# Optimization experiments

Hardware: AMD Instinct MI355X
Metric: run time of the kernel (lower is better)

## Reference

```python
import jax, jax.numpy as jnp
import numpy as np

TOP_K = 3
THRESH = 0.2
# scales=[1] -> multi_scale_fft reduces to one full-length window:
# combined_amplitudes = |rfft(x, axis=1)|.mean(channels)

def setup_inputs() -> dict:
    key = jax.random.key(0)
    x = jax.random.normal(key, (64, 4096, 64), dtype=jnp.float32)
    return {"x": x}

def _autocorr_score(xi, p):
    # xi: [T, C]; p: scalar int32 period (guaranteed in [2, T//2]).
    # Equivalent to mean over consecutive period-segments i of
    # cosine_similarity(flatten(seg_i), flatten(seg_{i+1})) — computed via
    # prefix sums of lag-p cross products so the segment reshape never needs
    # a data-dependent shape.
    T, C = xi.shape
    t = jnp.arange(T)
    tp = t + p
    m = (tp < T).astype(xi.dtype)
    xs = xi[jnp.clip(tp, 0, T - 1)]                  # [T, C] rows shifted by p
    r = (xi * xs).sum(-1) * m                        # <x[t], x[t+p]>
    q = (xi * xi).sum(-1)                            # ||x[t]||^2
    z = jnp.zeros((1,), xi.dtype)
    CR = jnp.concatenate([z, jnp.cumsum(r)])         # [T+1]
    CQ = jnp.concatenate([z, jnp.cumsum(q)])
    nper = T // p
    i = jnp.arange(T // 2)                           # max possible segments (p>=2)
    seg = i < (nper - 1)
    s = jnp.clip(i * p, 0, T)
    e = jnp.clip((i + 1) * p, 0, T)
    e2 = jnp.clip((i + 2) * p, 0, T)
    dots = CR[e] - CR[s]                             # flat dot(seg_i, seg_{i+1})
    na = jnp.sqrt(jnp.maximum(CQ[e] - CQ[s], 0.0))
    nb = jnp.sqrt(jnp.maximum(CQ[e2] - CQ[e], 0.0))
    cos = dots / jnp.maximum(na * nb, 1e-8)          # F.cosine_similarity eps
    denom = jnp.maximum(nper - 1, 1).astype(xi.dtype)
    score = jnp.where(seg, cos, 0.0).sum() / denom
    return jnp.where(nper >= 2, score, 0.0)

def reference(x):
    B, T, C = x.shape
    half = T // 2
    # multi-scale FFT with scales=[1]: single window == full sequence
    amps = jnp.abs(jnp.fft.rfft(x, axis=1)).mean(-1)       # [B, T//2+1]
    _, idx = jax.lax.top_k(amps, 2 * TOP_K)                 # [B, 2K]
    period_f = T / (idx + 1).astype(jnp.float32)            # candidate periods
    in_range = (period_f >= 2.0) & (period_f <= half)       # float-period filter
    p_int = jnp.clip(jnp.floor(period_f).astype(jnp.int32), 2, half)
    pf_floor = jnp.floor(period_f)
    in_range_int = (pf_floor >= 2.0) & (pf_floor <= half)   # int-period filter
    # autocorrelation validation score per (batch, candidate)
    scores = jax.vmap(lambda xi, ps: jax.vmap(lambda p: _autocorr_score(xi, p))(ps))(x, p_int)  # [B, 2K]
    valid = in_range & in_range_int & (scores > THRESH)
    # deterministic fallback periods (torch.randint branch unreachable for TOP_K=3)
    common = np.array([T // 4, T // 3, T // 2, int(T / 1.5)], dtype=np.int32)
    common = common[(common >= 2) & (common <= half)]
    add = jnp.asarray(common)                               # [>= TOP_K]

    def select(p_row, v_row):
        order = jnp.argsort(jnp.logical_not(v_row), stable=True)  # valid first, order kept
        sp = p_row[order][:TOP_K]
        cnt = jnp.minimum(v_row.sum(), TOP_K)
        j = jnp.arange(TOP_K)
        filled = jnp.where(j < cnt, sp, add[jnp.clip(j - cnt, 0, add.shape[0] - 1)])
        w = jnp.where(j < cnt, 1.0, 0.5)
        return filled.astype(jnp.float32), w.astype(jnp.float32)

    periods, weights = jax.vmap(select)(p_int, valid)       # [B, TOP_K] each
    return periods, weights
```

## Files before the change

kernel.cpp:

```cpp
#include <hip/hip_runtime.h>
#include <math.h>

#define T_LEN 4096
#define C_CH 64
#define B_N 64
#define NBINS 2049
#define K2 6
#define TOPK 3
#define THRESH_V 0.2f

#define PIDX(i) ((i) + ((i) >> 5))
#define ZSZ (T_LEN + (T_LEN >> 5))

__device__ __forceinline__ unsigned short f2bf(float v) {
    unsigned int u = __float_as_uint(v);
    u += 0x7FFFu + ((u >> 16) & 1u);
    return (unsigned short)(u >> 16);
}
__device__ __forceinline__ float bf2f(unsigned short h) {
    return __uint_as_float(((unsigned int)h) << 16);
}

__device__ __forceinline__ float2 cmul(float2 a, float2 b) {
    return make_float2(a.x * b.x - a.y * b.y, a.x * b.y + a.y * b.x);
}
__device__ __forceinline__ float2 cadd(float2 a, float2 b) { return make_float2(a.x + b.x, a.y + b.y); }
__device__ __forceinline__ float2 csub(float2 a, float2 b) { return make_float2(a.x - b.x, a.y - b.y); }

__device__ __forceinline__ void dft16(float2* v) {
    const float C2 = 0.70710678118654752f;
    const float C1 = 0.92387953251128676f;
    const float S1 = 0.38268343236508977f;
    const int br[16] = {0, 8, 4, 12, 2, 10, 6, 14, 1, 9, 5, 13, 3, 11, 7, 15};
    float2 a[16];
#pragma unroll
    for (int i = 0; i < 16; ++i) a[i] = v[br[i]];
#pragma unroll
    for (int g = 0; g < 16; g += 2) {
        float2 t = a[g + 1];
        a[g + 1] = csub(a[g], t);
        a[g] = cadd(a[g], t);
    }
#pragma unroll
    for (int g = 0; g < 16; g += 4) {
        {
            float2 t = a[g + 2];
            a[g + 2] = csub(a[g], t);
            a[g] = cadd(a[g], t);
        }
        {
            float2 t = make_float2(a[g + 3].y, -a[g + 3].x);
            a[g + 3] = csub(a[g + 1], t);
            a[g + 1] = cadd(a[g + 1], t);
        }
    }
    {
        const float2 W4[4] = {{1.f, 0.f}, {C2, -C2}, {0.f, -1.f}, {-C2, -C2}};
#pragma unroll
        for (int g = 0; g < 16; g += 8)
#pragma unroll
            for (int j = 0; j < 4; ++j) {
                float2 t = cmul(W4[j], a[g + 4 + j]);
                a[g + 4 + j] = csub(a[g + j], t);
                a[g + j] = cadd(a[g + j], t);
            }
    }
    {
        const float2 W8[8] = {{1.f, 0.f}, {C1, -S1}, {C2, -C2}, {S1, -C1},
                              {0.f, -1.f}, {-S1, -C1}, {-C2, -C2}, {-C1, -S1}};
#pragma unroll
        for (int j = 0; j < 8; ++j) {
            float2 t = cmul(W8[j], a[8 + j]);
            a[8 + j] = csub(a[j], t);
            a[j] = cadd(a[j], t);
        }
    }
#pragma unroll
    for (int i = 0; i < 16; ++i) v[i] = a[i];
}

__global__ void transpose_cvt_kernel(const float* __restrict__ x,
                                     unsigned short* __restrict__ xtbf,
                                     float* __restrict__ amps) {
    __shared__ float tile[64][65];
    const int b = blockIdx.y;
    const int t0 = blockIdx.x * 64;
    const int lane = threadIdx.x & 63;
    const int w = threadIdx.x >> 6;
    {
        const int blin = blockIdx.y * (T_LEN / 64) + blockIdx.x;
        if (threadIdx.x < 34) {
            int idx = blin * 34 + threadIdx.x;
            if (idx < B_N * NBINS) amps[idx] = 0.f;
        }
    }
    const float* xb = x + (size_t)b * T_LEN * C_CH;
#pragma unroll
    for (int i = 0; i < 16; ++i) {
        int r = w * 16 + i;
        tile[r][lane] = xb[(size_t)(t0 + r) * C_CH + lane];
    }
    __syncthreads();
    const int half = lane >> 5;
    const int tc = (lane & 31) * 2;
#pragma unroll
    for (int it = 0; it < 8; ++it) {
        int c = it * 8 + w * 2 + half;
        float v0 = tile[tc][c];
        float v1 = tile[tc + 1][c];
        unsigned int o = (unsigned int)f2bf(v0) | ((unsigned int)f2bf(v1) << 16);
        unsigned int* dst = (unsigned int*)(xtbf + ((size_t)b * C_CH + c) * T_LEN + t0);
        dst[lane & 31] = o;
    }
}

template <int MODE>
__global__ void fft_amp_kernel(const void* __restrict__ srcv, float* __restrict__ amps) {
    __shared__ float2 Z[ZSZ];
    const int pair = blockIdx.x;
    const int b = blockIdx.y;
    const int tid = threadIdx.x;

    if (MODE == 0) {
        const unsigned short* r0 =
            (const unsigned short*)srcv + ((size_t)b * C_CH + pair * 2) * T_LEN;
        const unsigned short* r1 = r0 + T_LEN;
#pragma unroll
        for (int k = 0; k < 2; ++k) {
            int t0 = k * 2048 + tid * 8;
            uint4 u0 = *(const uint4*)(r0 + t0);
            uint4 u1 = *(const uint4*)(r1 + t0);
            unsigned int a[4] = {u0.x, u0.y, u0.z, u0.w};
            unsigned int c[4] = {u1.x, u1.y, u1.z, u1.w};
#pragma unroll
            for (int j = 0; j < 4; ++j) {
                Z[PIDX(t0 + 2 * j)] = make_float2(__uint_as_float(a[j] << 16),
                                                  __uint_as_float(c[j] << 16));
                Z[PIDX(t0 + 2 * j + 1)] = make_float2(__uint_as_float(a[j] & 0xFFFF0000u),
                                                      __uint_as_float(c[j] & 0xFFFF0000u));
            }
        }
    } else {
        const float* x = (const float*)srcv;
        const int c0 = pair * 2;
        for (int t = tid; t < T_LEN; t += 256)
            Z[PIDX(t)] = *(const float2*)(x + ((size_t)b * T_LEN + t) * C_CH + c0);
    }
    __syncthreads();

    {
        float2 v[16];
#pragma unroll
        for (int t = 0; t < 16; ++t) v[t] = Z[PIDX(tid + 256 * t)];
        dft16(v);
        float s, c;
        __sincosf(-(float)tid * 1.5339807878856412e-3f, &s, &c);
        float2 w1 = make_float2(c, s), w = w1;
#pragma unroll
        for (int r = 1; r < 16; ++r) {
            v[r] = cmul(v[r], w);
            w = cmul(w, w1);
        }
#pragma unroll
        for (int r = 0; r < 16; ++r) Z[PIDX(256 * r + tid)] = v[r];
    }
    __syncthreads();

    {
        const int r = tid >> 4, mu = tid & 15;
        float2 v[16];
#pragma unroll
        for (int nu = 0; nu < 16; ++nu) v[nu] = Z[PIDX(256 * r + mu + 16 * nu)];
        dft16(v);
        float s, c;
        __sincosf(-(float)mu * 2.4543692606170259e-2f, &s, &c);
        float2 w1 = make_float2(c, s), w = w1;
#pragma unroll
        for (int rho = 1; rho < 16; ++rho) {
            v[rho] = cmul(v[rho], w);
            w = cmul(w, w1);
        }
#pragma unroll
        for (int rho = 0; rho < 16; ++rho) Z[PIDX(256 * r + mu + 16 * rho)] = v[rho];
    }
    __builtin_amdgcn_wave_barrier();

    {
        const int r = tid >> 4, rho = tid & 15;
        float2 v[16];
#pragma unroll
        for (int mu = 0; mu < 16; ++mu) v[mu] = Z[PIDX(256 * r + mu + 16 * rho)];
        dft16(v);
#pragma unroll
        for (int mp = 0; mp < 16; ++mp) Z[PIDX(256 * r + mp + 16 * rho)] = v[mp];
    }
    __syncthreads();

    for (int k = tid; k < NBINS; k += 256) {
        int km = (T_LEN - k) & (T_LEN - 1);
        int sk = 256 * (k & 15) + 16 * ((k >> 4) & 15) + (k >> 8);
        int sm = 256 * (km & 15) + 16 * ((km >> 4) & 15) + (km >> 8);
        float2 zk = Z[PIDX(sk)];
        float2 zm = Z[PIDX(sm)];
        float ax = 0.5f * (zk.x + zm.x);
        float ay = 0.5f * (zk.y - zm.y);
        float bx = 0.5f * (zk.y + zm.y);
        float by = -0.5f * (zk.x - zm.x);
        float amp = sqrtf(ax * ax + ay * ay) + sqrtf(bx * bx + by * by);
        atomicAdd(&amps[(size_t)b * NBINS + k], amp);
    }
}

__global__ void topk_kernel(const float* __restrict__ amps, int* __restrict__ p_int,
                            int* __restrict__ preval) {
    __shared__ float vals[NBINS];
    __shared__ float sval[256];
    __shared__ int sidx[256];
    __shared__ int sel[K2];
    const int b = blockIdx.x;
    const int tid = threadIdx.x;
    for (int k = tid; k < NBINS; k += 256) vals[k] = amps[(size_t)b * NBINS + k];
    __syncthreads();
    for (int pass = 0; pass < K2; ++pass) {
        float bv = -INFINITY;
        int bi = NBINS;
        for (int k = tid; k < NBINS; k += 256) {
            float v = vals[k];
            if (v > bv || (v == bv && k < bi)) { bv = v; bi = k; }
        }
        sval[tid] = bv;
        sidx[tid] = bi;
        __syncthreads();
        for (int off = 128; off > 0; off >>= 1) {
            if (tid < off) {
                float ov = sval[tid + off];
                int oi = sidx[tid + off];
                if (ov > sval[tid] || (ov == sval[tid] && oi < sidx[tid])) {
                    sval[tid] = ov;
                    sidx[tid] = oi;
                }
            }
            __syncthreads();
        }
        if (tid == 0) {
            sel[pass] = sidx[0];
            vals[sidx[0]] = -INFINITY;
        }
        __syncthreads();
    }
    if (tid < K2) {
        int idx = sel[tid];
        float pf = (float)T_LEN / (float)(idx + 1);
        int ir = (pf >= 2.0f) && (pf <= (float)(T_LEN / 2));
        float pff = floorf(pf);
        int iri = (pff >= 2.0f) && (pff <= (float)(T_LEN / 2));
        int pi = (int)pff;
        pi = pi < 2 ? 2 : (pi > T_LEN / 2 ? T_LEN / 2 : pi);
        p_int[b * K2 + tid] = pi;
        preval[b * K2 + tid] = ir && iri;
    }
}

__global__ void rq_kernel(const unsigned short* __restrict__ xtbf,
                          const int* __restrict__ p_int, float* __restrict__ r_ws,
                          float* __restrict__ q_ws) {
    const int b = blockIdx.y;
    const int t = blockIdx.x * 64 + threadIdx.x;
    const unsigned short* xb = xtbf + (size_t)b * C_CH * T_LEN;

    int tpc[K2];
    float m[K2];
#pragma unroll
    for (int j = 0; j < K2; ++j) {
        int tp = t + p_int[b * K2 + j];
        m[j] = (tp < T_LEN) ? 1.f : 0.f;
        tpc[j] = (tp < T_LEN) ? tp : (T_LEN - 1);
    }

    float qacc = 0.f;
    float racc[K2] = {0.f, 0.f, 0.f, 0.f, 0.f, 0.f};
    for (int cc = 0; cc < C_CH; cc += 8) {
        float a[8];
        float bv[K2][8];
#pragma unroll
        for (int k = 0; k < 8; ++k) a[k] = bf2f(xb[(size_t)(cc + k) * T_LEN + t]);
#pragma unroll
        for (int j = 0; j < K2; ++j)
#pragma unroll
            for (int k = 0; k < 8; ++k)
                bv[j][k] = bf2f(xb[(size_t)(cc + k) * T_LEN + tpc[j]]);
#pragma unroll
        for (int k = 0; k < 8; ++k) {
            qacc += a[k] * a[k];
#pragma unroll
            for (int j = 0; j < K2; ++j) racc[j] += a[k] * bv[j][k];
        }
    }
    q_ws[(size_t)b * T_LEN + t] = qacc;
#pragma unroll
    for (int j = 0; j < K2; ++j)
        r_ws[((size_t)b * K2 + j) * T_LEN + t] = racc[j] * m[j];
}

__device__ __forceinline__ void block_scan2_4096(float* a, float* b, float* tsa, float* tsb,
                                                 int tid) {
    float la[16], lb[16];
    const int base = tid * 16;
    float sa = 0.f, sb = 0.f;
#pragma unroll
    for (int i = 0; i < 16; ++i) {
        sa += a[base + i];
        la[i] = sa;
        sb += b[base + i];
        lb[i] = sb;
    }
    tsa[tid] = sa;
    tsb[tid] = sb;
    __syncthreads();
    for (int off = 1; off < 256; off <<= 1) {
        float va = (tid >= off) ? tsa[tid - off] : 0.f;
        float vb = (tid >= off) ? tsb[tid - off] : 0.f;
        __syncthreads();
        tsa[tid] += va;
        tsb[tid] += vb;
        __syncthreads();
    }
    float offa = tsa[tid] - sa;
    float offb = tsb[tid] - sb;
#pragma unroll
    for (int i = 0; i < 16; ++i) {
        a[base + i] = offa + la[i];
        b[base + i] = offb + lb[i];
    }
    __syncthreads();
}

__device__ __forceinline__ void block_scan_4096(float* a, float* tsum, int tid) {
    float loc[16];
    const int base = tid * 16;
    float s = 0.f;
#pragma unroll
    for (int i = 0; i < 16; ++i) {
        s += a[base + i];
        loc[i] = s;
    }
    tsum[tid] = s;
    __syncthreads();
    for (int off = 1; off < 256; off <<= 1) {
        float v = (tid >= off) ? tsum[tid - off] : 0.f;
        __syncthreads();
        tsum[tid] += v;
        __syncthreads();
    }
    float offs = tsum[tid] - s;
#pragma unroll
    for (int i = 0; i < 16; ++i) a[base + i] = offs + loc[i];
    __syncthreads();
}

__global__ void score_kernel(const float* __restrict__ r_ws, const float* __restrict__ q_ws,
                             const int* __restrict__ p_int, float* __restrict__ scores) {
    __shared__ float r_s[T_LEN];
    __shared__ float q_s[T_LEN];
    __shared__ float tsum[512];
    const int cand = blockIdx.x;
    const int b = blockIdx.y;
    const int tid = threadIdx.x;
    const int p = p_int[b * K2 + cand];
    const float4* rsrc = (const float4*)(r_ws + ((size_t)b * K2 + cand) * T_LEN);
    const float4* qsrc = (const float4*)(q_ws + (size_t)b * T_LEN);
    for (int i = tid; i < T_LEN / 4; i += 256) {
        ((float4*)r_s)[i] = rsrc[i];
        ((float4*)q_s)[i] = qsrc[i];
    }
    __syncthreads();
    block_scan2_4096(r_s, q_s, tsum, tsum + 256, tid);
    const int nper = T_LEN / p;
    float part = 0.f;
    for (int i = tid; i < nper - 1; i += 256) {
        int s0 = i * p;
        int e = s0 + p;
        int e2 = e + p;
        float crs = s0 ? r_s[s0 - 1] : 0.f;
        float dots = r_s[e - 1] - crs;
        float cqs = s0 ? q_s[s0 - 1] : 0.f;
        float qa = q_s[e - 1] - cqs;
        float qb = q_s[e2 - 1] - q_s[e - 1];
        float na = sqrtf(fmaxf(qa, 0.f));
        float nb = sqrtf(fmaxf(qb, 0.f));
        part += dots / fmaxf(na * nb, 1e-8f);
    }
    tsum[tid] = part;
    __syncthreads();
    for (int off = 128; off > 0; off >>= 1) {
        if (tid < off) tsum[tid] += tsum[tid + off];
        __syncthreads();
    }
    if (tid == 0) scores[b * K2 + cand] = tsum[0] / (float)(nper - 1);
}

__global__ void autocorr_kernel(const float* __restrict__ x, const int* __restrict__ p_int,
                                float* __restrict__ scores) {
    __shared__ float r_s[T_LEN];
    __shared__ float q_s[T_LEN];
    __shared__ float tsum[256];
    const int cand = blockIdx.x;
    const int b = blockIdx.y;
    const int tid = threadIdx.x;
    const int p = p_int[b * K2 + cand];
    const float* xb = x + (size_t)b * T_LEN * C_CH;
    for (int t = tid; t < T_LEN; t += 256) {
        const float4* row = (const float4*)(xb + (size_t)t * C_CH);
        float q = 0.f, r = 0.f;
        if (t + p < T_LEN) {
            const float4* row2 = (const float4*)(xb + (size_t)(t + p) * C_CH);
#pragma unroll
            for (int i = 0; i < 16; ++i) {
                float4 a = row[i], c = row2[i];
                r += a.x * c.x + a.y * c.y + a.z * c.z + a.w * c.w;
                q += a.x * a.x + a.y * a.y + a.z * a.z + a.w * a.w;
            }
        } else {
#pragma unroll
            for (int i = 0; i < 16; ++i) {
                float4 a = row[i];
                q += a.x * a.x + a.y * a.y + a.z * a.z + a.w * a.w;
            }
        }
        r_s[t] = r;
        q_s[t] = q;
    }
    __syncthreads();
    block_scan_4096(r_s, tsum, tid);
    block_scan_4096(q_s, tsum, tid);
    const int nper = T_LEN / p;
    float part = 0.f;
    for (int i = tid; i < nper - 1; i += 256) {
        int s0 = i * p;
        int e = s0 + p;
        int e2 = e + p;
        float crs = s0 ? r_s[s0 - 1] : 0.f;
        float dots = r_s[e - 1] - crs;
        float cqs = s0 ? q_s[s0 - 1] : 0.f;
        float qa = q_s[e - 1] - cqs;
        float qb = q_s[e2 - 1] - q_s[e - 1];
        float na = sqrtf(fmaxf(qa, 0.f));
        float nb = sqrtf(fmaxf(qb, 0.f));
        part += dots / fmaxf(na * nb, 1e-8f);
    }
    tsum[tid] = part;
    __syncthreads();
    for (int off = 128; off > 0; off >>= 1) {
        if (tid < off) tsum[tid] += tsum[tid + off];
        __syncthreads();
    }
    if (tid == 0) scores[b * K2 + cand] = tsum[0] / (float)(nper - 1);
}

__global__ void select_kernel(const int* __restrict__ p_int, const int* __restrict__ preval,
                              const float* __restrict__ scores, float* __restrict__ out) {
    const int b = threadIdx.x;
    if (b >= B_N) return;
    int sel[TOPK];
    int cnt = 0;
    for (int j = 0; j < K2; ++j) {
        if (preval[b * K2 + j] && scores[b * K2 + j] > THRESH_V) {
            if (cnt < TOPK) sel[cnt] = p_int[b * K2 + j];
            cnt++;
        }
    }
    if (cnt > TOPK) cnt = TOPK;
    int add[4];
    int nadd = 0;
    int cms[4] = {T_LEN / 4, T_LEN / 3, T_LEN / 2, (int)((float)T_LEN / 1.5f)};
    for (int i = 0; i < 4; ++i)
        if (cms[i] >= 2 && cms[i] <= T_LEN / 2) add[nadd++] = cms[i];
    for (int j = 0; j < TOPK; ++j) {
        float pv, wv;
        if (j < cnt) {
            pv = (float)sel[j];
            wv = 1.0f;
        } else {
            int a = j - cnt;
            if (a > nadd - 1) a = nadd - 1;
            pv = (float)add[a];
            wv = 0.5f;
        }
        out[b * TOPK + j] = pv;
        out[B_N * TOPK + b * TOPK + j] = wv;
    }
}

static size_t align256(size_t v) { return (v + 255) & ~(size_t)255; }

extern "C" void kernel_launch(void* const* d_in, const int* in_sizes, int n_in,
                              void* d_out, int out_size, void* d_ws, size_t ws_size,
                              hipStream_t stream) {
    const float* x = (const float*)d_in[0];
    float* out = (float*)d_out;
    char* ws = (char*)d_ws;

    const size_t amps_b = align256((size_t)B_N * NBINS * sizeof(float));
    const size_t int_b = align256((size_t)B_N * K2 * sizeof(int));
    const size_t r_b = align256((size_t)B_N * K2 * T_LEN * sizeof(float));
    const size_t q_b = align256((size_t)B_N * T_LEN * sizeof(float));
    const size_t xtbf_b = align256((size_t)B_N * T_LEN * C_CH * sizeof(short));

    size_t off = 0;
    float* amps = (float*)(ws + off); off += amps_b;
    int* p_int = (int*)(ws + off); off += int_b;
    int* preval = (int*)(ws + off); off += int_b;
    float* scores = (float*)(ws + off); off += int_b;
    float* r_ws = (float*)(ws + off); off += r_b;
    float* q_ws = (float*)(ws + off); off += q_b;
    unsigned short* xtbf = (unsigned short*)(ws + off); off += xtbf_b;
    const size_t full_need = off;

    if (ws_size >= full_need) {
        transpose_cvt_kernel<<<dim3(T_LEN / 64, B_N), 256, 0, stream>>>(x, xtbf, amps);
        fft_amp_kernel<0><<<dim3(C_CH / 2, B_N), 256, 0, stream>>>(xtbf, amps);
        topk_kernel<<<B_N, 256, 0, stream>>>(amps, p_int, preval);
        rq_kernel<<<dim3(T_LEN / 64, B_N), 64, 0, stream>>>(xtbf, p_int, r_ws, q_ws);
        score_kernel<<<dim3(K2, B_N), 256, 0, stream>>>(r_ws, q_ws, p_int, scores);
        select_kernel<<<1, 64, 0, stream>>>(p_int, preval, scores, out);
    } else {
        hipMemsetAsync(amps, 0, amps_b, stream);
        fft_amp_kernel<1><<<dim3(C_CH / 2, B_N), 256, 0, stream>>>(x, amps);
        topk_kernel<<<B_N, 256, 0, stream>>>(amps, p_int, preval);
        autocorr_kernel<<<dim3(K2, B_N), 256, 0, stream>>>(x, p_int, scores);
        select_kernel<<<1, 64, 0, stream>>>(p_int, preval, scores, out);
    }
}
```

Measured before the change: 168.5 us.

## Store FFT shared buffer as packed bf16 and fuse select into score kernel

The FFT workspace in shared memory changes from float2 to packed bf16 pairs. This halves LDS use per block so more blocks can be resident, and a launch bound of 8 blocks per CU is added. The select kernel is folded into the score kernel: a global atomic counter lets the last finishing block do the final selection, which removes one launch. In exchange every FFT stage now rounds to bf16, which lowers precision and could change top-k picks, and the last-block pattern relies on atomics for memory ordering.

```diff
diff --git a/kernel.cpp b/kernel.cpp
--- a/kernel.cpp
+++ b/kernel.cpp
@@ -19,6 +19,12 @@
 }
 __device__ __forceinline__ float bf2f(unsigned short h) {
     return __uint_as_float(((unsigned int)h) << 16);
+}
+__device__ __forceinline__ float2 zld(unsigned int v) {
+    return make_float2(__uint_as_float(v << 16), __uint_as_float(v & 0xFFFF0000u));
+}
+__device__ __forceinline__ unsigned int zst(float2 z) {
+    return (unsigned int)f2bf(z.x) | ((unsigned int)f2bf(z.y) << 16);
 }
 
 __device__ __forceinline__ float2 cmul(float2 a, float2 b) {
@@ -115,8 +121,9 @@
 }
 
 template <int MODE>
+__launch_bounds__(256, 8)
 __global__ void fft_amp_kernel(const void* __restrict__ srcv, float* __restrict__ amps) {
-    __shared__ float2 Z[ZSZ];
+    __shared__ unsigned int Z[ZSZ];
     const int pair = blockIdx.x;
     const int b = blockIdx.y;
     const int tid = threadIdx.x;
@@ -134,24 +141,24 @@
             unsigned int c[4] = {u1.x, u1.y, u1.z, u1.w};
 #pragma unroll
             for (int j = 0; j < 4; ++j) {
-                Z[PIDX(t0 + 2 * j)] = make_float2(__uint_as_float(a[j] << 16),
-                                                  __uint_as_float(c[j] << 16));
-                Z[PIDX(t0 + 2 * j + 1)] = make_float2(__uint_as_float(a[j] & 0xFFFF0000u),
-                                                      __uint_as_float(c[j] & 0xFFFF0000u));
+                Z[PIDX(t0 + 2 * j)] = (a[j] & 0xFFFFu) | (c[j] << 16);
+                Z[PIDX(t0 + 2 * j + 1)] = (a[j] >> 16) | (c[j] & 0xFFFF0000u);
             }
         }
     } else {
         const float* x = (const float*)srcv;
         const int c0 = pair * 2;
-        for (int t = tid; t < T_LEN; t += 256)
-            Z[PIDX(t)] = *(const float2*)(x + ((size_t)b * T_LEN + t) * C_CH + c0);
+        for (int t = tid; t < T_LEN; t += 256) {
+            float2 v = *(const float2*)(x + ((size_t)b * T_LEN + t) * C_CH + c0);
+            Z[PIDX(t)] = zst(v);
+        }
     }
     __syncthreads();
 
     {
         float2 v[16];
 #pragma unroll
-        for (int t = 0; t < 16; ++t) v[t] = Z[PIDX(tid + 256 * t)];
+        for (int t = 0; t < 16; ++t) v[t] = zld(Z[PIDX(tid + 256 * t)]);
         dft16(v);
         float s, c;
         __sincosf(-(float)tid * 1.5339807878856412e-3f, &s, &c);
@@ -162,7 +169,7 @@
             w = cmul(w, w1);
         }
 #pragma unroll
-        for (int r = 0; r < 16; ++r) Z[PIDX(256 * r + tid)] = v[r];
+        for (int r = 0; r < 16; ++r) Z[PIDX(256 * r + tid)] = zst(v[r]);
     }
     __syncthreads();
 
@@ -170,7 +177,7 @@
         const int r = tid >> 4, mu = tid & 15;
         float2 v[16];
 #pragma unroll
-        for (int nu = 0; nu < 16; ++nu) v[nu] = Z[PIDX(256 * r + mu + 16 * nu)];
+        for (int nu = 0; nu < 16; ++nu) v[nu] = zld(Z[PIDX(256 * r + mu + 16 * nu)]);
         dft16(v);
         float s, c;
         __sincosf(-(float)mu * 2.4543692606170259e-2f, &s, &c);
@@ -181,7 +188,7 @@
             w = cmul(w, w1);
         }
 #pragma unroll
-        for (int rho = 0; rho < 16; ++rho) Z[PIDX(256 * r + mu + 16 * rho)] = v[rho];
+        for (int rho = 0; rho < 16; ++rho) Z[PIDX(256 * r + mu + 16 * rho)] = zst(v[rho]);
     }
     __builtin_amdgcn_wave_barrier();
 
@@ -189,10 +196,10 @@
         const int r = tid >> 4, rho = tid & 15;
         float2 v[16];
 #pragma unroll
-        for (int mu = 0; mu < 16; ++mu) v[mu] = Z[PIDX(256 * r + mu + 16 * rho)];
+        for (int mu = 0; mu < 16; ++mu) v[mu] = zld(Z[PIDX(256 * r + mu + 16 * rho)]);
         dft16(v);
 #pragma unroll
-        for (int mp = 0; mp < 16; ++mp) Z[PIDX(256 * r + mp + 16 * rho)] = v[mp];
+        for (int mp = 0; mp < 16; ++mp) Z[PIDX(256 * r + mp + 16 * rho)] = zst(v[mp]);
     }
     __syncthreads();
 
@@ -200,8 +207,8 @@
         int km = (T_LEN - k) & (T_LEN - 1);
         int sk = 256 * (k & 15) + 16 * ((k >> 4) & 15) + (k >> 8);
         int sm = 256 * (km & 15) + 16 * ((km >> 4) & 15) + (km >> 8);
-        float2 zk = Z[PIDX(sk)];
-        float2 zm = Z[PIDX(sm)];
+        float2 zk = zld(Z[PIDX(sk)]);
+        float2 zm = zld(Z[PIDX(sm)]);
         float ax = 0.5f * (zk.x + zm.x);
         float ay = 0.5f * (zk.y - zm.y);
         float bx = 0.5f * (zk.y + zm.y);
@@ -212,13 +219,14 @@
 }
 
 __global__ void topk_kernel(const float* __restrict__ amps, int* __restrict__ p_int,
-                            int* __restrict__ preval) {
+                            int* __restrict__ preval, int* __restrict__ counter) {
     __shared__ float vals[NBINS];
     __shared__ float sval[256];
     __shared__ int sidx[256];
     __shared__ int sel[K2];
     const int b = blockIdx.x;
     const int tid = threadIdx.x;
+    if (b == 0 && tid == 0) *counter = 0;
     for (int k = tid; k < NBINS; k += 256) vals[k] = amps[(size_t)b * NBINS + k];
     __syncthreads();
     for (int pass = 0; pass < K2; ++pass) {
@@ -358,11 +366,46 @@
     __syncthreads();
 }
 
+__device__ __forceinline__ void select_core(int b, const int* p_int, const int* preval,
+                                            const float* sc6, float* out) {
+    int sel[TOPK];
+    int cnt = 0;
+    for (int j = 0; j < K2; ++j) {
+        if (preval[b * K2 + j] && sc6[j] > THRESH_V) {
+            if (cnt < TOPK) sel[cnt] = p_int[b * K2 + j];
+            cnt++;
+        }
+    }
+    if (cnt > TOPK) cnt = TOPK;
+    int add[4];
+    int nadd = 0;
+    int cms[4] = {T_LEN / 4, T_LEN / 3, T_LEN / 2, (int)((float)T_LEN / 1.5f)};
+    for (int i = 0; i < 4; ++i)
+        if (cms[i] >= 2 && cms[i] <= T_LEN / 2) add[nadd++] = cms[i];
+    for (int j = 0; j < TOPK; ++j) {
+        float pv, wv;
+        if (j < cnt) {
+            pv = (float)sel[j];
+            wv = 1.0f;
+        } else {
+            int a = j - cnt;
+            if (a > nadd - 1) a = nadd - 1;
+            pv = (float)add[a];
+            wv = 0.5f;
+        }
+        out[b * TOPK + j] = pv;
+        out[B_N * TOPK + b * TOPK + j] = wv;
+    }
+}
+
 __global__ void score_kernel(const float* __restrict__ r_ws, const float* __restrict__ q_ws,
-                             const int* __restrict__ p_int, float* __restrict__ scores) {
+                             const int* __restrict__ p_int, const int* __restrict__ preval,
+                             float* __restrict__ scores, int* __restrict__ counter,
+                             float* __restrict__ out) {
     __shared__ float r_s[T_LEN];
     __shared__ float q_s[T_LEN];
     __shared__ float tsum[512];
+    __shared__ int lastflag;
     const int cand = blockIdx.x;
     const int b = blockIdx.y;
     const int tid = threadIdx.x;
@@ -396,7 +439,22 @@
         if (tid < off) tsum[tid] += tsum[tid + off];
         __syncthreads();
     }
-    if (tid == 0) scores[b * K2 + cand] = tsum[0] / (float)(nper - 1);
+    if (tid == 0) {
+        float sc = tsum[0] / (float)(nper - 1);
+        float old = atomicExch(&scores[b * K2 + cand], sc);
+        int inc;
+        asm volatile("v_mov_b32 %0, 1" : "=v"(inc) : "v"(old));
+        int prev = atomicAdd(counter, inc);
+        lastflag = (prev == K2 * B_N - 1) ? 1 : 0;
+    }
+    __syncthreads();
+    if (lastflag && tid < B_N) {
+        float sc6[K2];
+#pragma unroll
+        for (int j = 0; j < K2; ++j)
+            sc6[j] = atomicAdd(&scores[tid * K2 + j], 0.0f);
+        select_core(tid, p_int, preval, sc6, out);
+    }
 }
 
 __global__ void autocorr_kernel(const float* __restrict__ x, const int* __restrict__ p_int,
@@ -461,34 +519,9 @@
                               const float* __restrict__ scores, float* __restrict__ out) {
     const int b = threadIdx.x;
     if (b >= B_N) return;
-    int sel[TOPK];
-    int cnt = 0;
-    for (int j = 0; j < K2; ++j) {
-        if (preval[b * K2 + j] && scores[b * K2 + j] > THRESH_V) {
-            if (cnt < TOPK) sel[cnt] = p_int[b * K2 + j];
-            cnt++;
-        }
-    }
-    if (cnt > TOPK) cnt = TOPK;
-    int add[4];
-    int nadd = 0;
-    int cms[4] = {T_LEN / 4, T_LEN / 3, T_LEN / 2, (int)((float)T_LEN / 1.5f)};
-    for (int i = 0; i < 4; ++i)
-        if (cms[i] >= 2 && cms[i] <= T_LEN / 2) add[nadd++] = cms[i];
-    for (int j = 0; j < TOPK; ++j) {
-        float pv, wv;
-        if (j < cnt) {
-            pv = (float)sel[j];
-            wv = 1.0f;
-        } else {
-            int a = j - cnt;
-            if (a > nadd - 1) a = nadd - 1;
-            pv = (float)add[a];
-            wv = 0.5f;
-        }
-        out[b * TOPK + j] = pv;
-        out[B_N * TOPK + b * TOPK + j] = wv;
-    }
+    float sc6[K2];
+    for (int j = 0; j < K2; ++j) sc6[j] = scores[b * K2 + j];
+    select_core(b, p_int, preval, sc6, out);
 }
 
 static size_t align256(size_t v) { return (v + 255) & ~(size_t)255; }
@@ -511,6 +544,7 @@
     int* p_int = (int*)(ws + off); off += int_b;
     int* preval = (int*)(ws + off); off += int_b;
     float* scores = (float*)(ws + off); off += int_b;
+    int* counter = (int*)(ws + off); off += 256;
     float* r_ws = (float*)(ws + off); off += r_b;
     float* q_ws = (float*)(ws + off); off += q_b;
     unsigned short* xtbf = (unsigned short*)(ws + off); off += xtbf_b;
@@ -519,14 +553,14 @@
     if (ws_size >= full_need) {
         transpose_cvt_kernel<<<dim3(T_LEN / 64, B_N), 256, 0, stream>>>(x, xtbf, amps);
         fft_amp_kernel<0><<<dim3(C_CH / 2, B_N), 256, 0, stream>>>(xtbf, amps);
-        topk_kernel<<<B_N, 256, 0, stream>>>(amps, p_int, preval);
+        topk_kernel<<<B_N, 256, 0, stream>>>(amps, p_int, preval, counter);
         rq_kernel<<<dim3(T_LEN / 64, B_N), 64, 0, stream>>>(xtbf, p_int, r_ws, q_ws);
-        score_kernel<<<dim3(K2, B_N), 256, 0, stream>>>(r_ws, q_ws, p_int, scores);
-        select_kernel<<<1, 64, 0, stream>>>(p_int, preval, scores, out);
+        score_kernel<<<dim3(K2, B_N), 256, 0, stream>>>(r_ws, q_ws, p_int, preval, scores,
+                                                        counter, out);
     } else {
         hipMemsetAsync(amps, 0, amps_b, stream);
         fft_amp_kernel<1><<<dim3(C_CH / 2, B_N), 256, 0, stream>>>(x, amps);
-        topk_kernel<<<B_N, 256, 0, stream>>>(amps, p_int, preval);
+        topk_kernel<<<B_N, 256, 0, stream>>>(amps, p_int, preval, counter);
         autocorr_kernel<<<dim3(K2, B_N), 256, 0, stream>>>(x, p_int, scores);
         select_kernel<<<1, 64, 0, stream>>>(p_int, preval, scores, out);
     }
```

New measurement: 166.8 us. No clear change (-1.0%).
